# Performance work log

Hardware: AMD Instinct MI355X
Metric: run time of the kernel (lower is better)

## Reference

```python
import jax, jax.numpy as jnp
import numpy as np

D_MODEL = 2048
NUM_HEADS = 16
HEAD_DIM = D_MODEL // NUM_HEADS  # 128
BASE = 10000.0


def rotate_half(x):
    x1, x2 = x[..., : x.shape[-1] // 2], x[..., x.shape[-1] // 2 :]
    return jnp.concatenate((-x2, x1), axis=-1)


def setup_inputs() -> dict:
    key = jax.random.key(0)
    ks = jax.random.split(key, 9)
    B, S, D = 2, 2048, D_MODEL
    s = 1.0 / np.sqrt(D)
    return {
        "x": jax.random.normal(ks[0], (B, S, D), dtype=jnp.float32),
        "Wq": jax.random.normal(ks[1], (D, D), dtype=jnp.float32) * s,
        "bq": jnp.zeros((D,), dtype=jnp.float32),
        "Wk": jax.random.normal(ks[2], (D, D), dtype=jnp.float32) * s,
        "bk": jnp.zeros((D,), dtype=jnp.float32),
        "Wv": jax.random.normal(ks[3], (D, D), dtype=jnp.float32) * s,
        "bv": jnp.zeros((D,), dtype=jnp.float32),
        "Wo": jax.random.normal(ks[4], (D, D), dtype=jnp.float32) * s,
        "bo": jnp.zeros((D,), dtype=jnp.float32),
    }


def reference(x, Wq, bq, Wk, bk, Wv, bv, Wo, bo):
    B, S, D = x.shape
    H, hd = NUM_HEADS, HEAD_DIM

    def proj(W, b):
        # nn.Linear: x @ W^T + b, then split heads -> [B, H, S, hd]
        return (x @ W.T + b).reshape(B, S, H, hd).transpose(0, 2, 1, 3)

    q = proj(Wq, bq)
    k = proj(Wk, bk)
    v = proj(Wv, bv)

    # Rotary embedding table (note: original applies cos()/sin() to a
    # tensor that already contains [sin(si), cos(si)] — reproduced faithfully).
    positions = jnp.arange(S, dtype=jnp.float32)
    inv_freq = 1.0 / (BASE ** (jnp.arange(0, hd, 2, dtype=jnp.float32) / hd))
    sinusoid = positions[:, None] * inv_freq[None, :]            # [S, hd/2]
    emb = jnp.concatenate((jnp.sin(sinusoid), jnp.cos(sinusoid)), axis=-1)  # [S, hd]
    cos_e = jnp.cos(emb)  # broadcast over [B, H, S, hd]
    sin_e = jnp.sin(emb)

    q_rot = q * cos_e + rotate_half(q) * sin_e
    k_rot = k * cos_e + rotate_half(k) * sin_e

    scale = 1.0 / jnp.sqrt(jnp.asarray(hd, dtype=x.dtype))
    attn = jnp.einsum("bhqd,bhkd->bhqk", q_rot, k_rot) * scale
    attn = jax.nn.softmax(attn, axis=-1)
    out = jnp.einsum("bhqk,bhkd->bhqd", attn, v)
    out = out.transpose(0, 2, 1, 3).reshape(B, S, D)
    return out @ Wo.T + bo
```

## Files before the change

### kernel.cpp

```cpp
#include <hip/hip_runtime.h>
#include <math.h>

#define D_MODEL 2048
#define NHEADS  16
#define HD      128
#define SEQ     2048
#define BATCH   2
#define SCALE   0.08838834764831845f
#define SMAX    20.0f

typedef __attribute__((ext_vector_type(8))) short short8;
typedef __attribute__((ext_vector_type(4))) float f32x4;

#define MFMA16(a,b,c) __builtin_amdgcn_mfma_f32_16x16x32_bf16((a),(b),(c),0,0,0)

__device__ __forceinline__ unsigned short f2bf(float x){
    unsigned u = __float_as_uint(x);
    return (unsigned short)((u + 0x7FFFu + ((u>>16)&1u)) >> 16);
}
__device__ __forceinline__ float bf2f(unsigned short h){ return __uint_as_float(((unsigned)h)<<16); }

__device__ __forceinline__ void async16(void* lds, const void* g){
    __builtin_amdgcn_global_load_lds((const __attribute__((address_space(1))) unsigned int*)g,
                                     (__attribute__((address_space(3))) unsigned int*)lds, 16, 0, 0);
}

__device__ __forceinline__ void split4(float4 v, ushort4* h, ushort4* l){
    h->x=f2bf(v.x); l->x=f2bf(v.x-bf2f(h->x));
    h->y=f2bf(v.y); l->y=f2bf(v.y-bf2f(h->y));
    h->z=f2bf(v.z); l->z=f2bf(v.z-bf2f(h->z));
    h->w=f2bf(v.w); l->w=f2bf(v.w-bf2f(h->w));
}

__global__ __launch_bounds__(256)
void prep_all(const float* __restrict__ x, const float* __restrict__ Wq,
              const float* __restrict__ Wk, const float* __restrict__ Wv,
              unsigned short* __restrict__ Xhi, unsigned short* __restrict__ Xlo,
              unsigned short* __restrict__ WqHi, unsigned short* __restrict__ WqLo,
              unsigned short* __restrict__ WkHi, unsigned short* __restrict__ WkLo,
              unsigned short* __restrict__ WvHi,
              float4* __restrict__ tab)
{
    const int b = blockIdx.x, t = threadIdx.x;
    if (b < 8192) {
        int i = b*256 + t;
        ushort4 h,l; split4(((const float4*)x)[i], &h, &l);
        ((ushort4*)Xhi)[i]=h; ((ushort4*)Xlo)[i]=l;
    } else if (b < 12288) {
        int i = (b-8192)*256 + t;
        ushort4 h,l; split4(((const float4*)Wq)[i], &h, &l);
        ((ushort4*)WqHi)[i]=h; ((ushort4*)WqLo)[i]=l;
    } else if (b < 16384) {
        int i = (b-12288)*256 + t;
        ushort4 h,l; split4(((const float4*)Wk)[i], &h, &l);
        ((ushort4*)WkHi)[i]=h; ((ushort4*)WkLo)[i]=l;
    } else if (b < 20480) {
        int i = (b-16384)*256 + t;
        ushort4 h,l; split4(((const float4*)Wv)[i], &h, &l);
        ((ushort4*)WvHi)[i]=h;
    } else {
        int i = (b-20480)*256 + t;
        int s = i >> 6, d = i & 63;
        float f = powf(10000.0f, -(float)d * (1.0f/64.0f));
        float sv = (float)s * f;
        float sn = sinf(sv), cs = cosf(sv);
        tab[i] = (float4){cosf(sn), sinf(sn), cosf(cs), sinf(cs)};
    }
}

__global__ __launch_bounds__(256)
void split_w(const float* __restrict__ src, unsigned short* __restrict__ hi,
             unsigned short* __restrict__ lo, int n4)
{
    int i = blockIdx.x*256 + threadIdx.x;
    if (i >= n4) return;
    ushort4 h,l; split4(((const float4*)src)[i], &h, &l);
    ((ushort4*)hi)[i]=h; ((ushort4*)lo)[i]=l;
}


template<bool THREE, int Q>
__device__ __forceinline__ void phase_mfma(const unsigned short* Bh, const unsigned short* Bl,
                                           const short8 (&ah)[4], const short8 (&al)[4],
                                           f32x4 (&acc)[4][4], int wn, int quad, int l15)
{
    int n = wn*64 + Q*16 + l15;
    int c = (quad ^ ((n>>1)&3))*8;
    short8 bh_ = *(const short8*)&Bh[n*32 + c];
    short8 bl_ = {};
    if constexpr (THREE) bl_ = *(const short8*)&Bl[n*32 + c];
    __builtin_amdgcn_s_setprio(1);
    acc[0][Q] = MFMA16(ah[0], bh_, acc[0][Q]);
    acc[1][Q] = MFMA16(ah[1], bh_, acc[1][Q]);
    acc[2][Q] = MFMA16(ah[2], bh_, acc[2][Q]);
    acc[3][Q] = MFMA16(ah[3], bh_, acc[3][Q]);
    acc[0][Q] = MFMA16(al[0], bh_, acc[0][Q]);
    acc[1][Q] = MFMA16(al[1], bh_, acc[1][Q]);
    acc[2][Q] = MFMA16(al[2], bh_, acc[2][Q]);
    acc[3][Q] = MFMA16(al[3], bh_, acc[3][Q]);
    if constexpr (THREE) {
        acc[0][Q] = MFMA16(ah[0], bl_, acc[0][Q]);
        acc[1][Q] = MFMA16(ah[1], bl_, acc[1][Q]);
        acc[2][Q] = MFMA16(ah[2], bl_, acc[2][Q]);
        acc[3][Q] = MFMA16(ah[3], bl_, acc[3][Q]);
    }
    __builtin_amdgcn_s_setprio(0);
}

template<bool THREE>
__device__ __forceinline__ void gemm_core_r1(const unsigned short* __restrict__ Agh,
                                             const unsigned short* __restrict__ Agl,
                                             const unsigned short* __restrict__ Bgh,
                                             const unsigned short* __restrict__ Bgl,
                                             unsigned short* lds, int m0, int n0,
                                             f32x4 (&acc)[4][4])
{
    const int t = threadIdx.x, w = t>>6, lane = t&63;
    const int quad = lane>>4, l15 = lane&15;
    const int wm = w>>1, wn = w&1;

    unsigned short *c0 = lds, *c1 = lds + 24576, *c2 = lds + 49152;

    auto stageA = [&](unsigned short* P, const unsigned short* SRC, int u, int kt2){
        int idx = t + u*512; int rw = idx>>2, sg = idx&3;
        int sgp = sg ^ ((rw>>1)&3);
        async16((char*)(P + rw*32 + sg*8), SRC + (size_t)(m0+rw)*2048 + kt2 + sgp*8);
    };
    auto stageB = [&](unsigned short* P, const unsigned short* SRC, int kt2){
        int rw = t>>2, sg = t&3; int sgp = sg ^ ((rw>>1)&3);
        async16((char*)(P + rw*32 + sg*8), SRC + (size_t)(n0+rw)*2048 + kt2 + sgp*8);
    };

    stageA(c0,        Agh, 0, 0);  stageA(c0,        Agh, 1, 0);
    stageA(c0+8192,   Agl, 0, 0);  stageA(c0+8192,   Agl, 1, 0);
    stageB(c0+16384,  Bgh, 0);
    if constexpr (THREE) stageB(c0+20480, Bgl, 0);
    stageA(c1,        Agh, 0, 32); stageA(c1,        Agh, 1, 32);
    stageA(c1+8192,   Agl, 0, 32); stageA(c1+8192,   Agl, 1, 32);
    stageB(c1+16384,  Bgh, 32);
    if constexpr (THREE) stageB(c1+20480, Bgl, 32);

    for (int kt = 0; kt < 64; ++kt) {
        if (kt == 63) {
            asm volatile("s_waitcnt vmcnt(0)" ::: "memory");
        } else if constexpr (THREE) {
            asm volatile("s_waitcnt vmcnt(6)" ::: "memory");
        } else {
            asm volatile("s_waitcnt vmcnt(5)" ::: "memory");
        }
        __builtin_amdgcn_s_barrier();
        __builtin_amdgcn_sched_barrier(0);

        const unsigned short* Ah = c0;
        const unsigned short* Al = c0 + 8192;
        const unsigned short* Bh = c0 + 16384;
        const unsigned short* Bl = c0 + 20480;
        const int  kt2 = (kt+2)*32;
        const bool st  = (kt < 62);

        short8 ah[4], al[4];
#pragma unroll
        for (int mi=0;mi<4;mi++){
            int m = wm*64 + mi*16 + l15;
            int c = (quad ^ ((m>>1)&3))*8;
            ah[mi] = *(const short8*)&Ah[m*32 + c];
            al[mi] = *(const short8*)&Al[m*32 + c];
        }
        if (st){ stageA(c2,       Agh, 0, kt2); stageA(c2,       Agh, 1, kt2); }
        phase_mfma<THREE,0>(Bh, Bl, ah, al, acc, wn, quad, l15);
        __builtin_amdgcn_s_barrier();

        if (st){ stageA(c2+8192,  Agl, 0, kt2); stageA(c2+8192,  Agl, 1, kt2); }
        phase_mfma<THREE,1>(Bh, Bl, ah, al, acc, wn, quad, l15);
        __builtin_amdgcn_s_barrier();

        if (st){ stageB(c2+16384, Bgh, kt2); }
        phase_mfma<THREE,2>(Bh, Bl, ah, al, acc, wn, quad, l15);
        __builtin_amdgcn_s_barrier();

        if constexpr (THREE) { if (st) stageB(c2+20480, Bgl, kt2); }
        phase_mfma<THREE,3>(Bh, Bl, ah, al, acc, wn, quad, l15);
        __builtin_amdgcn_s_barrier();

        unsigned short* tmp = c0; c0 = c1; c1 = c2; c2 = tmp;
    }
}

template<bool THREE>
__device__ __forceinline__ void read_A3(const unsigned short* Ah, const unsigned short* Al,
                                        short8 (&ah)[4], short8 (&al)[4],
                                        int wm, int quad, int l15)
{
#pragma unroll
    for (int mi=0;mi<4;mi++){
        int m = wm*64 + mi*16 + l15;
        int c = (quad ^ ((m>>1)&3))*8;
        ah[mi] = *(const short8*)&Ah[m*32 + c];
        al[mi] = *(const short8*)&Al[m*32 + c];
    }
}

template<bool THREE, int Q>
__device__ __forceinline__ void read_B3(const unsigned short* Bh, const unsigned short* Bl,
                                        short8& bh, short8& bl, int wn, int quad, int l15)
{
    int n = wn*64 + Q*16 + l15;
    int c = (quad ^ ((n>>1)&3))*8;
    bh = *(const short8*)&Bh[n*32 + c];
    if constexpr (THREE) bl = *(const short8*)&Bl[n*32 + c];
    else                 bl = (short8){};
}

template<bool THREE, int Q>
__device__ __forceinline__ void col_mfma3(const short8 (&ah)[4], const short8 (&al)[4],
                                          short8 bh, short8 bl, f32x4 (&acc)[4][4])
{
    __builtin_amdgcn_s_setprio(1);
    acc[0][Q] = MFMA16(ah[0], bh, acc[0][Q]);
    acc[1][Q] = MFMA16(ah[1], bh, acc[1][Q]);
    acc[2][Q] = MFMA16(ah[2], bh, acc[2][Q]);
    acc[3][Q] = MFMA16(ah[3], bh, acc[3][Q]);
    acc[0][Q] = MFMA16(al[0], bh, acc[0][Q]);
    acc[1][Q] = MFMA16(al[1], bh, acc[1][Q]);
    acc[2][Q] = MFMA16(al[2], bh, acc[2][Q]);
    acc[3][Q] = MFMA16(al[3], bh, acc[3][Q]);
    if constexpr (THREE) {
        acc[0][Q] = MFMA16(ah[0], bl, acc[0][Q]);
        acc[1][Q] = MFMA16(ah[1], bl, acc[1][Q]);
        acc[2][Q] = MFMA16(ah[2], bl, acc[2][Q]);
        acc[3][Q] = MFMA16(ah[3], bl, acc[3][Q]);
    }
    __builtin_amdgcn_s_setprio(0);
}

template<bool THREE>
__device__ __forceinline__ void gemm_core3(const unsigned short* __restrict__ Agh,
                                           const unsigned short* __restrict__ Agl,
                                           const unsigned short* __restrict__ Bgh,
                                           const unsigned short* __restrict__ Bgl,
                                           unsigned short* lds, int m0, int n0,
                                           f32x4 (&acc)[4][4])
{
    const int t = threadIdx.x, w = t>>6, lane = t&63;
    const int quad = lane>>4, l15 = lane&15;
    const int wm = w>>1, wn = w&1;

    unsigned short *c0 = lds, *c1 = lds + 24576, *c2 = lds + 49152;

    auto stageA = [&](unsigned short* P, const unsigned short* SRC, int u, int kt2){
        int idx = t + u*512; int rw = idx>>2, sg = idx&3;
        int sgp = sg ^ ((rw>>1)&3);
        async16((char*)(P + rw*32 + sg*8), SRC + (size_t)(m0+rw)*2048 + kt2 + sgp*8);
    };
    auto stageB = [&](unsigned short* P, const unsigned short* SRC, int kt2){
        int rw = t>>2, sg = t&3; int sgp = sg ^ ((rw>>1)&3);
        async16((char*)(P + rw*32 + sg*8), SRC + (size_t)(n0+rw)*2048 + kt2 + sgp*8);
    };
    auto stage_tile = [&](unsigned short* P, int kt2){
        stageA(P,        Agh, 0, kt2);  stageA(P,        Agh, 1, kt2);
        stageA(P+8192,   Agl, 0, kt2);  stageA(P+8192,   Agl, 1, kt2);
        stageB(P+16384,  Bgh, kt2);
        if constexpr (THREE) stageB(P+20480, Bgl, kt2);
    };

    stage_tile(c0, 0);
    stage_tile(c1, 32);
    if constexpr (THREE) asm volatile("s_waitcnt vmcnt(6)" ::: "memory");
    else                 asm volatile("s_waitcnt vmcnt(5)" ::: "memory");
    __builtin_amdgcn_s_barrier();
    __builtin_amdgcn_sched_barrier(0);

    short8 ah[4], al[4], ahp[4], alp[4];
    short8 b0h, b0l, b1h, b1l, b2h, b2l, b3h, b3l, b0hp, b0lp;
    read_A3<THREE>(c0, c0+8192, ah, al, wm, quad, l15);
    read_B3<THREE,0>(c0+16384, c0+20480, b0h, b0l, wn, quad, l15);

    for (int kt = 0; kt < 64; ++kt) {
        const bool st  = (kt < 62);
        const int  kt2 = (kt+2)*32;

        read_B3<THREE,1>(c0+16384, c0+20480, b1h, b1l, wn, quad, l15);
        if (st){ stageA(c2,       Agh, 0, kt2); stageA(c2,       Agh, 1, kt2); }
        col_mfma3<THREE,0>(ah, al, b0h, b0l, acc);
        __builtin_amdgcn_sched_barrier(0);

        read_B3<THREE,2>(c0+16384, c0+20480, b2h, b2l, wn, quad, l15);
        if (st){ stageA(c2+8192,  Agl, 0, kt2); stageA(c2+8192,  Agl, 1, kt2); }
        col_mfma3<THREE,1>(ah, al, b1h, b1l, acc);
        __builtin_amdgcn_sched_barrier(0);

        read_B3<THREE,3>(c0+16384, c0+20480, b3h, b3l, wn, quad, l15);
        if (st){ stageB(c2+16384, Bgh, kt2); }
        col_mfma3<THREE,2>(ah, al, b2h, b2l, acc);
        __builtin_amdgcn_sched_barrier(0);

        if constexpr (THREE) { if (st) stageB(c2+20480, Bgl, kt2); }
        if (kt < 63) {
            __builtin_amdgcn_sched_barrier(0);
            asm volatile("s_waitcnt lgkmcnt(0)" ::: "memory");
            if (st) {
                if constexpr (THREE) asm volatile("s_waitcnt vmcnt(6)" ::: "memory");
                else                 asm volatile("s_waitcnt vmcnt(5)" ::: "memory");
            } else {
                asm volatile("s_waitcnt vmcnt(0)" ::: "memory");
            }
            __builtin_amdgcn_s_barrier();
            __builtin_amdgcn_sched_barrier(0);
            read_A3<THREE>(c1, c1+8192, ahp, alp, wm, quad, l15);
            read_B3<THREE,0>(c1+16384, c1+20480, b0hp, b0lp, wn, quad, l15);
            __builtin_amdgcn_sched_barrier(0);
            col_mfma3<THREE,3>(ah, al, b3h, b3l, acc);
#pragma unroll
            for (int i=0;i<4;i++){ ah[i]=ahp[i]; al[i]=alp[i]; }
            b0h = b0hp; b0l = b0lp;
            unsigned short* tmp = c0; c0 = c1; c1 = c2; c2 = tmp;
        } else {
            col_mfma3<THREE,3>(ah, al, b3h, b3l, acc);
        }
    }
}

__global__ __launch_bounds__(512,2)
void gemm_qkv(const unsigned short* __restrict__ Xhi_g, const unsigned short* __restrict__ Xlo_g,
              const unsigned short* __restrict__ wsplit,
              const float* __restrict__ bq, const float* __restrict__ bk,
              const float* __restrict__ bv,
              const float4* __restrict__ tab,
              unsigned short* __restrict__ Qhi, unsigned short* __restrict__ Qlo,
              unsigned short* __restrict__ Khi, unsigned short* __restrict__ Klo,
              unsigned short* __restrict__ Vt)
{
    extern __shared__ unsigned short ldsm[];
    const int z = blockIdx.z;
    const int t = threadIdx.x, w = t>>6, lane = t&63;
    const int quad = lane>>4, l15 = lane&15;
    const int wm = w>>1, wn = w&1;
    const int m0 = blockIdx.y*256, n0 = blockIdx.x*128;

    f32x4 acc[4][4];
#pragma unroll
    for (int i=0;i<4;i++)
#pragma unroll
        for (int j=0;j<4;j++) acc[i][j] = (f32x4){0.f,0.f,0.f,0.f};

    if (z < 2) {
        const unsigned short* Whi = wsplit + (size_t)z*8388608u;
        const unsigned short* Wlo = Whi + 4194304u;

        gemm_core3<true>(Xhi_g, Xlo_g, Whi, Wlo, ldsm, m0, n0, acc);
        __syncthreads();

        const float* bias = (z==0)?bq:bk;
#pragma unroll
        for (int ni=0;ni<4;ni++){
            float bv_ = bias[n0 + wn*64 + ni*16 + l15];
#pragma unroll
            for (int mi=0;mi<4;mi++){
                acc[mi][ni][0]+=bv_; acc[mi][ni][1]+=bv_; acc[mi][ni][2]+=bv_; acc[mi][ni][3]+=bv_;
            }
        }

        float* xch = (float*)ldsm;
        unsigned short* OHi = (z==0)?Qhi:Khi;
        unsigned short* OLo = (z==0)?Qlo:Klo;
        const float scl = (z==0)?SCALE:1.0f;
        const int h = blockIdx.x;
        const int b = m0>>11;
        const size_t bhbase = ((size_t)(b*16+h)*2048);

        if (wn == 0) {
#pragma unroll
            for (int mi=0;mi<4;mi++)
#pragma unroll
            for (int ni=2;ni<4;ni++)
#pragma unroll
            for (int r=0;r<4;r++)
                xch[(wm*64+mi*16+quad*4+r)*68 + (ni-2)*16+l15] = acc[mi][ni][r];
        } else {
#pragma unroll
            for (int mi=0;mi<4;mi++)
#pragma unroll
            for (int ni=0;ni<2;ni++)
#pragma unroll
            for (int r=0;r<4;r++)
                xch[(wm*64+mi*16+quad*4+r)*68 + 32 + ni*16+l15] = acc[mi][ni][r];
        }
        __syncthreads();

        if (wn == 0) {
#pragma unroll
            for (int ni2=0;ni2<2;ni2++){
                int d = ni2*16 + l15;
#pragma unroll
                for (int mi=0;mi<4;mi++)
#pragma unroll
                for (int r=0;r<4;r++){
                    int ml = wm*64 + mi*16 + quad*4 + r;
                    int s = (m0 + ml) & 2047;
                    float4 tv = tab[s*64 + d];
                    float c_lo = acc[mi][ni2][r];
                    float c_hi = xch[ml*68 + 32 + d];
                    float o1 = (c_lo*tv.x - c_hi*tv.y)*scl;
                    float o2 = (c_hi*tv.z + c_lo*tv.w)*scl;
                    size_t base = (bhbase + s)*128;
                    unsigned short h1=f2bf(o1); OHi[base+d]=h1;    OLo[base+d]=f2bf(o1-bf2f(h1));
                    unsigned short h2=f2bf(o2); OHi[base+64+d]=h2; OLo[base+64+d]=f2bf(o2-bf2f(h2));
                }
            }
        } else {
#pragma unroll
            for (int ni2=0;ni2<2;ni2++){
                int d = 32 + ni2*16 + l15;
#pragma unroll
                for (int mi=0;mi<4;mi++)
#pragma unroll
                for (int r=0;r<4;r++){
                    int ml = wm*64 + mi*16 + quad*4 + r;
                    int s = (m0 + ml) & 2047;
                    float4 tv = tab[s*64 + d];
                    float c_lo = xch[ml*68 + (d-32)];
                    float c_hi = acc[mi][ni2+2][r];
                    float o1 = (c_lo*tv.x - c_hi*tv.y)*scl;
                    float o2 = (c_hi*tv.z + c_lo*tv.w)*scl;
                    size_t base = (bhbase + s)*128;
                    unsigned short h1=f2bf(o1); OHi[base+d]=h1;    OLo[base+d]=f2bf(o1-bf2f(h1));
                    unsigned short h2=f2bf(o2); OHi[base+64+d]=h2; OLo[base+64+d]=f2bf(o2-bf2f(h2));
                }
            }
        }
    } else {
        const unsigned short* WvHi = wsplit + 16777216u;

        gemm_core_r1<false>(Xhi_g, Xlo_g, WvHi, nullptr, ldsm, m0, n0, acc);
        __syncthreads();

#pragma unroll
        for (int ni=0;ni<4;ni++){
            float bv_ = bv[n0 + wn*64 + ni*16 + l15];
#pragma unroll
            for (int mi=0;mi<4;mi++){
                acc[mi][ni][0]+=bv_; acc[mi][ni][1]+=bv_; acc[mi][ni][2]+=bv_; acc[mi][ni][3]+=bv_;
            }
        }

        unsigned short* vb = ldsm;
#pragma unroll
        for (int mi=0;mi<4;mi++)
#pragma unroll
        for (int ni=0;ni<4;ni++)
#pragma unroll
        for (int r=0;r<4;r++){
            int d  = wn*64 + ni*16 + l15;
            int ml = wm*64 + mi*16 + quad*4 + r;
            vb[d*264 + ml] = f2bf(acc[mi][ni][r]);
        }
        __syncthreads();

        const int b = m0>>11, s0 = m0&2047, h = blockIdx.x;
        unsigned short* vdst = Vt + (size_t)(b*16+h)*128*2048;
        const int dr = t>>2, part = (t&3)*64;
#pragma unroll
        for (int j=0;j<8;j++){
            uint4 v = *(const uint4*)&vb[dr*264 + part + j*8];
            *(uint4*)(vdst + (size_t)dr*2048 + s0 + part + j*8) = v;
        }
    }
}

__global__ __launch_bounds__(512,2)
void gemm_o(const unsigned short* __restrict__ Ahi_g, const unsigned short* __restrict__ Alo_g,
            const unsigned short* __restrict__ Whi_g, const unsigned short* __restrict__ Wlo_g,
            const float* __restrict__ bias, float* __restrict__ out)
{
    extern __shared__ unsigned short ldsm[];
    const int t = threadIdx.x, w = t>>6, lane = t&63;
    const int quad = lane>>4, l15 = lane&15;
    const int wm = w>>1, wn = w&1;
    const int m0 = blockIdx.y*256, n0 = blockIdx.x*128;

    f32x4 acc[4][4];
#pragma unroll
    for (int i=0;i<4;i++)
#pragma unroll
        for (int j=0;j<4;j++) acc[i][j] = (f32x4){0.f,0.f,0.f,0.f};

    gemm_core_r1<true>(Ahi_g, Alo_g, Whi_g, Wlo_g, ldsm, m0, n0, acc);

#pragma unroll
    for (int ni=0;ni<4;ni++){
        int n = n0 + wn*64 + ni*16 + l15;
        float bv_ = bias[n];
#pragma unroll
        for (int mi=0;mi<4;mi++)
#pragma unroll
        for (int r=0;r<4;r++){
            int m = m0 + wm*64 + mi*16 + quad*4 + r;
            out[(size_t)m*2048 + n] = acc[mi][ni][r] + bv_;
        }
    }
}

__global__ __launch_bounds__(256,2)
void flash_mfma(const unsigned short* __restrict__ Qhi, const unsigned short* __restrict__ Qlo,
                const unsigned short* __restrict__ Khi, const unsigned short* __restrict__ Klo,
                const unsigned short* __restrict__ Vt,
                unsigned short* __restrict__ Ohi, unsigned short* __restrict__ Olo)
{
    const int t=threadIdx.x, w=t>>6, lane=t&63, quad=lane>>4, l15=lane&15;
    const int bh = blockIdx.y, qt = blockIdx.x;

    __shared__ __align__(16) unsigned short sm[32768];
    unsigned short* Ps = sm + 24576 + w*2048;

    short8 qf[2][2][4];
    const size_t qrow = (size_t)bh*2048 + qt*128 + w*32;
#pragma unroll
    for (int mb=0;mb<2;mb++){
        size_t r = qrow + mb*16 + l15;
#pragma unroll
        for (int kc=0;kc<4;kc++){
            qf[0][mb][kc] = *(const short8*)(Qhi + r*128 + kc*32 + quad*8);
            qf[1][mb][kc] = *(const short8*)(Qlo + r*128 + kc*32 + quad*8);
        }
    }

    f32x4 O[2][8];
#pragma unroll
    for (int mb=0;mb<2;mb++)
#pragma unroll
        for (int nb=0;nb<8;nb++) O[mb][nb]=(f32x4){0.f,0.f,0.f,0.f};
    float lrow[2][4];
#pragma unroll
    for (int mb=0;mb<2;mb++)
#pragma unroll
        for (int r=0;r<4;r++) lrow[mb][r]=0.f;

    const char* KhiB = (const char*)(Khi + (size_t)bh*2048*128);
    const char* KloB = (const char*)(Klo + (size_t)bh*2048*128);
    const unsigned short* VtB = Vt + (size_t)bh*128*2048;
    char* smb = (char*)sm;

    for (int kt=0; kt<2048; kt+=64) {
#pragma unroll
        for (int i=0;i<4;i++){
            int o16 = t + 256*i;
            int krow = o16>>4, kc = o16&15;
            int kcp = kc ^ (krow&15);
            async16(smb + i*4096 + t*16,         KhiB + (size_t)kt*256 + krow*256 + kcp*16);
            async16(smb + 16384 + i*4096 + t*16, KloB + (size_t)kt*256 + krow*256 + kcp*16);
            int d = (t>>3) + i*32, c = t&7;
            int cp = c ^ (d&7);
            async16(smb + 32768 + i*4096 + t*16, VtB + (size_t)d*2048 + kt + cp*8);
        }
        __syncthreads();

        f32x4 S[2][4];
#pragma unroll
        for (int mb=0;mb<2;mb++)
#pragma unroll
            for (int nb=0;nb<4;nb++) S[mb][nb]=(f32x4){0.f,0.f,0.f,0.f};
#pragma unroll
        for (int kc=0;kc<4;kc++)
#pragma unroll
        for (int nb=0;nb<4;nb++){
            int m = nb*16+l15;
            int c = ((kc*4+quad) ^ (m&15))*8;
            short8 kh = *(const short8*)&sm[m*128 + c];
            short8 kl = *(const short8*)&sm[8192 + m*128 + c];
#pragma unroll
            for (int mb=0;mb<2;mb++){
                S[mb][nb] = MFMA16(qf[0][mb][kc], kh, S[mb][nb]);
                S[mb][nb] = MFMA16(qf[1][mb][kc], kh, S[mb][nb]);
                S[mb][nb] = MFMA16(qf[0][mb][kc], kl, S[mb][nb]);
            }
        }

#pragma unroll
        for (int mb=0;mb<2;mb++)
#pragma unroll
        for (int nb=0;nb<4;nb++)
#pragma unroll
        for (int r=0;r<4;r++){
            float p = __expf(S[mb][nb][r] - SMAX);
            lrow[mb][r] += p;
            int q = mb*16 + quad*4 + r;
            int c = nb*16 + l15;
            Ps[q*64 + (((c>>3)^(q&7))<<3) + (c&7)] = f2bf(p);
        }

#pragma unroll
        for (int kc2=0;kc2<2;kc2++){
            short8 pf0 = *(const short8*)&Ps[(l15)*64      + (((kc2*4+quad)^(l15&7))<<3)];
            short8 pf1 = *(const short8*)&Ps[(16+l15)*64   + (((kc2*4+quad)^(l15&7))<<3)];
#pragma unroll
            for (int nb=0;nb<8;nb++){
                int d = nb*16+l15;
                int c = ((kc2*4+quad) ^ (d&7))*8;
                short8 vf = *(const short8*)&sm[16384 + d*64 + c];
                O[0][nb] = MFMA16(pf0, vf, O[0][nb]);
                O[1][nb] = MFMA16(pf1, vf, O[1][nb]);
            }
        }
        __syncthreads();
    }

#pragma unroll
    for (int mb=0;mb<2;mb++)
#pragma unroll
        for (int d=1;d<16;d<<=1)
#pragma unroll
            for (int r=0;r<4;r++) lrow[mb][r] += __shfl_xor(lrow[mb][r], d);

    const int b = bh>>4, h = bh&15;
#pragma unroll
    for (int mb=0;mb<2;mb++)
#pragma unroll
    for (int nb=0;nb<8;nb++)
#pragma unroll
    for (int r=0;r<4;r++){
        float v = O[mb][nb][r] / lrow[mb][r];
        int qg = qt*128 + w*32 + mb*16 + quad*4 + r;
        size_t base = ((size_t)(b*2048 + qg))*2048 + h*128 + nb*16 + l15;
        unsigned short hh = f2bf(v);
        Ohi[base]=hh; Olo[base]=f2bf(v-bf2f(hh));
    }
}

extern "C" void kernel_launch(void* const* d_in, const int* in_sizes, int n_in,
                              void* d_out, int out_size, void* d_ws, size_t ws_size,
                              hipStream_t stream)
{
    (void)in_sizes; (void)n_in; (void)out_size; (void)ws_size;
    const float* x  = (const float*)d_in[0];
    const float* Wq = (const float*)d_in[1];
    const float* bq = (const float*)d_in[2];
    const float* Wk = (const float*)d_in[3];
    const float* bk = (const float*)d_in[4];
    const float* Wv = (const float*)d_in[5];
    const float* bv = (const float*)d_in[6];
    const float* Wo = (const float*)d_in[7];
    const float* bo = (const float*)d_in[8];
    float* out = (float*)d_out;

    unsigned short* wsB = (unsigned short*)d_ws;
    unsigned short* C0  = wsB + 20971520u;
    unsigned short* Qhi = C0;
    unsigned short* Qlo = C0 + 8388608u;
    unsigned short* Khi = C0 + 16777216u;
    unsigned short* Klo = C0 + 25165824u;
    unsigned short* Vt  = C0 + 33554432u;
    float4* tab = (float4*)(wsB + 62914560u);

    unsigned short* Xhi = (unsigned short*)d_out;
    unsigned short* Xlo = Xhi + 8388608u;

    static bool attr_done = false;
    if (!attr_done) {
        (void)hipFuncSetAttribute(reinterpret_cast<const void*>(&gemm_qkv),
                                  hipFuncAttributeMaxDynamicSharedMemorySize, 147456);
        (void)hipFuncSetAttribute(reinterpret_cast<const void*>(&gemm_o),
                                  hipFuncAttributeMaxDynamicSharedMemorySize, 147456);
        attr_done = true;
    }

    prep_all<<<20992,256,0,stream>>>(x, Wq, Wk, Wv,
                                     Xhi, Xlo,
                                     wsB,            wsB+4194304u,
                                     wsB+8388608u,   wsB+12582912u,
                                     wsB+16777216u,  tab);

    gemm_qkv<<<dim3(16,16,3),512,147456,stream>>>(Xhi, Xlo, wsB, bq, bk, bv, tab,
                                                  Qhi, Qlo, Khi, Klo, Vt);

    unsigned short* Ohi = wsB;
    unsigned short* Olo = wsB + 8388608u;
    flash_mfma<<<dim3(16,32),256,0,stream>>>(Qhi,Qlo,Khi,Klo,Vt, Ohi, Olo);

    unsigned short* WoHi = C0;
    unsigned short* WoLo = C0 + 4194304u;
    split_w<<<4096,256,0,stream>>>(Wo, WoHi, WoLo, 1048576);

    gemm_o<<<dim3(16,16),512,147456,stream>>>(Ohi, Olo, WoHi, WoLo, bo, out);
}
```

Before: 631.1 us.

## Double-buffer flash attention K/V tiles with 32-key blocks and async prefetch

Splits the flash attention KV loop into 32-key tiles and keeps two LDS buffers, issuing the async global-to-LDS loads for the next tile before computing on the current one. This hides global load latency behind the MFMA work and replaces two syncthreads per iteration with one wait plus barrier. The smaller tile halves the P scratch and keeps total LDS within budget, at the cost of twice as many loop iterations and barriers.

```diff
diff --git a/kernel.cpp b/kernel.cpp
--- a/kernel.cpp
+++ b/kernel.cpp
@@ -509,8 +509,8 @@
     const int t=threadIdx.x, w=t>>6, lane=t&63, quad=lane>>4, l15=lane&15;
     const int bh = blockIdx.y, qt = blockIdx.x;
 
-    __shared__ __align__(16) unsigned short sm[32768];
-    unsigned short* Ps = sm + 24576 + w*2048;
+    __shared__ __align__(16) unsigned short sm[28672];
+    unsigned short* Ps = sm + 24576 + w*1024;
 
     short8 qf[2][2][4];
     const size_t qrow = (size_t)bh*2048 + qt*128 + w*32;
@@ -540,33 +540,48 @@
     const unsigned short* VtB = Vt + (size_t)bh*128*2048;
     char* smb = (char*)sm;
 
-    for (int kt=0; kt<2048; kt+=64) {
-#pragma unroll
-        for (int i=0;i<4;i++){
+    auto stage = [&](int buf, int kv){
+        char* base = smb + buf;
+#pragma unroll
+        for (int i=0;i<2;i++){
             int o16 = t + 256*i;
             int krow = o16>>4, kc = o16&15;
             int kcp = kc ^ (krow&15);
-            async16(smb + i*4096 + t*16,         KhiB + (size_t)kt*256 + krow*256 + kcp*16);
-            async16(smb + 16384 + i*4096 + t*16, KloB + (size_t)kt*256 + krow*256 + kcp*16);
-            int d = (t>>3) + i*32, c = t&7;
-            int cp = c ^ (d&7);
-            async16(smb + 32768 + i*4096 + t*16, VtB + (size_t)d*2048 + kt + cp*8);
-        }
-        __syncthreads();
-
-        f32x4 S[2][4];
+            async16(base + o16*16,        KhiB + (size_t)(kv+krow)*256 + kcp*16);
+            async16(base + 8192 + o16*16, KloB + (size_t)(kv+krow)*256 + kcp*16);
+            int d = o16>>2, cc = o16&3;
+            int cp = cc ^ (d&3);
+            async16(base + 16384 + o16*16, (const char*)(VtB + (size_t)d*2048 + kv + cp*8));
+        }
+    };
+
+    stage(0, 0);
+    int cur = 0;
+
+    for (int it = 0; it < 64; ++it) {
+        asm volatile("s_waitcnt vmcnt(0)" ::: "memory");
+        __builtin_amdgcn_s_barrier();
+        __builtin_amdgcn_sched_barrier(0);
+
+        if (it < 63) stage(cur ^ 24576, (it+1)*32);
+
+        const unsigned short* Kh = (const unsigned short*)(smb + cur);
+        const unsigned short* Kl = (const unsigned short*)(smb + cur + 8192);
+        const unsigned short* Vs = (const unsigned short*)(smb + cur + 16384);
+
+        f32x4 S[2][2];
 #pragma unroll
         for (int mb=0;mb<2;mb++)
 #pragma unroll
-            for (int nb=0;nb<4;nb++) S[mb][nb]=(f32x4){0.f,0.f,0.f,0.f};
+            for (int nb=0;nb<2;nb++) S[mb][nb]=(f32x4){0.f,0.f,0.f,0.f};
 #pragma unroll
         for (int kc=0;kc<4;kc++)
 #pragma unroll
-        for (int nb=0;nb<4;nb++){
+        for (int nb=0;nb<2;nb++){
             int m = nb*16+l15;
             int c = ((kc*4+quad) ^ (m&15))*8;
-            short8 kh = *(const short8*)&sm[m*128 + c];
-            short8 kl = *(const short8*)&sm[8192 + m*128 + c];
+            short8 kh = *(const short8*)&Kh[m*128 + c];
+            short8 kl = *(const short8*)&Kl[m*128 + c];
 #pragma unroll
             for (int mb=0;mb<2;mb++){
                 S[mb][nb] = MFMA16(qf[0][mb][kc], kh, S[mb][nb]);
@@ -578,30 +593,30 @@
 #pragma unroll
         for (int mb=0;mb<2;mb++)
 #pragma unroll
-        for (int nb=0;nb<4;nb++)
+        for (int nb=0;nb<2;nb++)
 #pragma unroll
         for (int r=0;r<4;r++){
             float p = __expf(S[mb][nb][r] - SMAX);
             lrow[mb][r] += p;
             int q = mb*16 + quad*4 + r;
             int c = nb*16 + l15;
-            Ps[q*64 + (((c>>3)^(q&7))<<3) + (c&7)] = f2bf(p);
-        }
-
-#pragma unroll
-        for (int kc2=0;kc2<2;kc2++){
-            short8 pf0 = *(const short8*)&Ps[(l15)*64      + (((kc2*4+quad)^(l15&7))<<3)];
-            short8 pf1 = *(const short8*)&Ps[(16+l15)*64   + (((kc2*4+quad)^(l15&7))<<3)];
-#pragma unroll
-            for (int nb=0;nb<8;nb++){
-                int d = nb*16+l15;
-                int c = ((kc2*4+quad) ^ (d&7))*8;
-                short8 vf = *(const short8*)&sm[16384 + d*64 + c];
-                O[0][nb] = MFMA16(pf0, vf, O[0][nb]);
-                O[1][nb] = MFMA16(pf1, vf, O[1][nb]);
-            }
-        }
-        __syncthreads();
+            Ps[q*32 + (((c>>3)^(q&3))<<3) + (c&7)] = f2bf(p);
+        }
+
+        short8 pf0 = *(const short8*)&Ps[l15*32      + ((quad^(l15&3))<<3)];
+        short8 pf1 = *(const short8*)&Ps[(16+l15)*32 + ((quad^(l15&3))<<3)];
+#pragma unroll
+        for (int nb=0;nb<8;nb++){
+            int d = nb*16+l15;
+            int c = (quad ^ (d&3))*8;
+            short8 vf = *(const short8*)&Vs[d*32 + c];
+            O[0][nb] = MFMA16(pf0, vf, O[0][nb]);
+            O[1][nb] = MFMA16(pf1, vf, O[1][nb]);
+        }
+
+        asm volatile("s_waitcnt lgkmcnt(0)" ::: "memory");
+        __builtin_amdgcn_sched_barrier(0);
+        cur ^= 24576;
     }
 
 #pragma unroll
```

Result: no change. 622.1 us, median of 2 (-1.4%).
